# Optimization experiments

Measured on AMD Instinct MI355X. Metric: run time of the kernel, lower is better.

## Reference

```python
import jax, jax.numpy as jnp
import numpy as np


def setup_inputs() -> dict:
    key = jax.random.key(0)
    k1, k2, k3 = jax.random.split(key, 3)
    B, N, M, D = 4, 1024, 2048, 9
    outputs = jax.random.normal(k1, (B, N, D), dtype=jnp.float32)
    targets = jax.random.normal(k2, (B, M, D), dtype=jnp.float32)
    mask = jax.random.randint(k3, (B, M), 0, 2).astype(bool)
    return {"outputs": outputs, "targets": targets, "mask": mask, "k": 64, "max_pair": 1024}


def reference(outputs, targets, mask, k, max_pair):
    # outputs: (B, N, 9), targets: (B, M, 9), mask: (B, M) bool
    y_pred = outputs[:, :max_pair]
    B, N, D = y_pred.shape
    M = targets.shape[1]

    # Statistics over masked ground-truth rows (weighted, jit-friendly)
    w = mask.astype(y_pred.dtype)            # (B, M)
    S = w.sum()                               # number of valid rows
    mean = jnp.einsum('bm,bmd->d', w, targets) / S               # (9,)
    centered = (targets - mean) * w[..., None]                    # (B, M, 9)
    cov = jnp.einsum('bmd,bme->de', centered, centered) / (S - 1.0)
    cov_inv = jnp.linalg.pinv(cov)                                # (9, 9)

    def maha(x):
        # NOTE: original code subtracts the GT mean from the pairwise
        # differences before the quadratic form -- kept faithfully.
        xc = x - mean
        return jnp.einsum('...i,ij,...j->...', xc, cov_inv, xc)

    def topk_smallest_per_col(d, kk):
        # d: (R, N); torch.topk(dim=0, largest=False) -> smallest kk per column
        return -jax.lax.top_k(-d.T, kk)[0]    # (N, kk)

    # Intra loss: GT-vs-pred pairwise distances, masked rows only
    diff = targets[:, :, None, :] - y_pred[:, None, :, :]          # (B, M, N, 9)
    Dn = maha(diff)                                                 # (B, M, N)
    Dn = jnp.where(mask[:, :, None], Dn, jnp.inf).reshape(B * M, N)
    intra_loss = topk_smallest_per_col(Dn, k).mean()

    # Inter (regularization) loss: pred-vs-pred pairwise
    # y_reg1_expand[b,i,j] = y_pred[b,j]; y_reg2_expand[b,i,j] = y_pred[b,i]
    diff_r = y_pred[:, None, :, :] - y_pred[:, :, None, :]          # (B, N, N, 9)
    Dr = maha(diff_r).reshape(B * N, N)
    inter_loss = topk_smallest_per_col(Dr, k).mean()

    return intra_loss - 0.1 * inter_loss
```

## Files before the change

### kernel.cpp

```cpp
#include <hip/hip_runtime.h>
#include <math.h>

#define B_ 4
#define N_ 1024
#define M_ 2048
#define D_ 9
#define K_ 64
#define BM_ (B_*M_)
#define BN_ (B_*N_)
#define TPRE_STRIDE 12
#define PPRE_STRIDE 12
#define NPART 32
#define NSTAT 55
#define TSEL 512

#define WS_A 0
#define WS_MEAN 81
#define WS_TPRE 96
#define WS_PPRE (WS_TPRE + BM_*TPRE_STRIDE)
#define WS_CS_INTRA (WS_PPRE + BN_*PPRE_STRIDE)
#define WS_CS_INTER (WS_CS_INTRA + N_)
#define WS_PART (WS_CS_INTER + N_)
#define WS_CANDI (WS_PART + NPART*(NSTAT+1))
#define WS_CANDE (WS_CANDI + 1024*1024)

__device__ __forceinline__ unsigned f2key(float f) {
  unsigned b = __float_as_uint(f);
  return (b & 0x80000000u) ? ~b : (b | 0x80000000u);
}
__device__ __forceinline__ float key2f(unsigned k) {
  unsigned b = (k & 0x80000000u) ? (k ^ 0x80000000u) : ~k;
  return __uint_as_float(b);
}

__device__ int detect_mask_fmt(const void* mask, int* flags ) {
  int tid = threadIdx.x;
  if (tid < 2) flags[tid] = 0;
  __syncthreads();
  const unsigned char* mb = (const unsigned char*)mask;
  int la = 0, lb = 0;
  for (int i = tid; i < BM_; i += blockDim.x) {
    unsigned char c = mb[i];
    if (c) { if (i & 3) la = 1; else if ((i & 7) == 4) lb = 1; }
  }
  if (la) atomicOr(&flags[0], 1);
  if (lb) atomicOr(&flags[1], 1);
  __syncthreads();
  return flags[0] ? 0 : (flags[1] ? 1 : 2);
}
__device__ __forceinline__ int mask_at(const void* mask, int fmt, int t) {
  if (fmt == 0) return ((const unsigned char*)mask)[t] != 0;
  if (fmt == 1) return ((const int*)mask)[t] != 0;
  return ((const long long*)mask)[t] != 0LL;
}

__global__ __launch_bounds__(256) void stats_part_kernel(
    const float* __restrict__ targets, const void* __restrict__ mask,
    float* __restrict__ ws) {
  __shared__ int flags[2];
  __shared__ float wpart[4][NSTAT];
  int tid = threadIdx.x;
  int fmt = detect_mask_fmt(mask, flags);
  int t = blockIdx.x * 256 + tid;

  float v[NSTAT];
  float tv[D_];
  int m = mask_at(mask, fmt, t);
  const float* tp = targets + t * D_;
#pragma unroll
  for (int d = 0; d < D_; ++d) tv[d] = m ? tp[d] : 0.f;
  v[0] = m ? 1.f : 0.f;
#pragma unroll
  for (int d = 0; d < D_; ++d) v[1 + d] = tv[d];
  {
    int p = 10;
#pragma unroll
    for (int i = 0; i < D_; ++i)
#pragma unroll
      for (int j = i; j < D_; ++j, ++p) v[p] = tv[i] * tv[j];
  }
#pragma unroll
  for (int off = 32; off > 0; off >>= 1)
#pragma unroll
    for (int p = 0; p < NSTAT; ++p) v[p] += __shfl_down(v[p], off);
  int wave = tid >> 6, lane = tid & 63;
  if (lane == 0)
#pragma unroll
    for (int p = 0; p < NSTAT; ++p) wpart[wave][p] = v[p];
  __syncthreads();
  if (tid < NSTAT) {
    float s = wpart[0][tid] + wpart[1][tid] + wpart[2][tid] + wpart[3][tid];
    ws[WS_PART + blockIdx.x * (NSTAT + 1) + tid] = s;
  }
}

__global__ __launch_bounds__(64) void stats_fin_kernel(float* __restrict__ ws) {
  __shared__ float tot[NSTAT];
  __shared__ float Atmp[9][9];
  int lane = threadIdx.x;
  if (lane < NSTAT) {
    double s = 0.0;
    for (int b = 0; b < NPART; ++b)
      s += (double)ws[WS_PART + b * (NSTAT + 1) + lane];
    tot[lane] = (float)s;
  }
  __syncthreads();
  float S = tot[0];
  float col[9];
  int j = lane - 9;
  if (lane < 9) {
    float mj = tot[1 + lane] / S;
#pragma unroll
    for (int r = 0; r < 9; ++r) {
      float mr = tot[1 + r] / S;
      int i0 = r < lane ? r : lane;
      int j0 = r < lane ? lane : r;
      int p = i0 * 9 - (i0 * (i0 - 1)) / 2 + (j0 - i0);
      col[r] = (tot[10 + p] - S * mr * mj) / (S - 1.0f);
    }
  } else {
#pragma unroll
    for (int r = 0; r < 9; ++r) col[r] = (r == j) ? 1.f : 0.f;
  }
#pragma unroll
  for (int c = 0; c < 9; ++c) {
    float pv = __shfl(col[c], c);
    float inv = 1.f / pv;
    col[c] *= inv;
    float f[9];
#pragma unroll
    for (int r = 0; r < 9; ++r) f[r] = __shfl(col[r], c);
#pragma unroll
    for (int r = 0; r < 9; ++r)
      if (r != c) col[r] -= f[r] * col[c];
  }
  if (lane >= 9 && lane < 18) {
#pragma unroll
    for (int r = 0; r < 9; ++r) Atmp[r][j] = col[r];
  }
  __syncthreads();
  if (lane < 9) ws[WS_MEAN + lane] = tot[1 + lane] / S;
  for (int idx = lane; idx < 81; idx += 64) {
    int i0 = idx / 9, j0 = idx % 9;
    ws[WS_A + idx] = 0.5f * (Atmp[i0][j0] + Atmp[j0][i0]);
  }
}

__global__ __launch_bounds__(256) void pre_kernel(
    const float* __restrict__ outputs, const float* __restrict__ targets,
    const void* __restrict__ mask, float* __restrict__ ws) {
  __shared__ int flags[2];
  __shared__ float Ash[81];
  __shared__ float msh[D_];
  int tid = threadIdx.x;
  int fmt = detect_mask_fmt(mask, flags);
  if (tid < 81) Ash[tid] = ws[WS_A + tid];
  if (tid < D_) msh[tid] = ws[WS_MEAN + tid];
  __syncthreads();
  int idx = blockIdx.x * 256 + tid;
  if (idx < BM_) {
    const float* tp = targets + idx * D_;
    float u[D_];
#pragma unroll
    for (int d = 0; d < D_; ++d) u[d] = tp[d] - msh[d];
    float cu = 0.f; float au[D_];
#pragma unroll
    for (int i = 0; i < D_; ++i) {
      float s = 0.f;
#pragma unroll
      for (int j = 0; j < D_; ++j) s += Ash[i * D_ + j] * u[j];
      au[i] = s; cu += u[i] * s;
    }
    if (!mask_at(mask, fmt, idx)) cu = INFINITY;
    float* o = ws + WS_TPRE + idx * TPRE_STRIDE;
#pragma unroll
    for (int d = 0; d < D_; ++d) o[d] = au[d];
    o[9] = cu; o[10] = 0.f; o[11] = 0.f;
  } else if (idx < BM_ + BN_) {
    int r = idx - BM_;
    const float* yp = outputs + r * D_;
    float y[D_], q[D_], aq[D_];
#pragma unroll
    for (int d = 0; d < D_; ++d) { y[d] = yp[d]; q[d] = y[d] + msh[d]; }
    float cp = 0.f, cq = 0.f;
#pragma unroll
    for (int i = 0; i < D_; ++i) {
      float sy = 0.f, sq = 0.f;
#pragma unroll
      for (int j = 0; j < D_; ++j) {
        sy += Ash[i * D_ + j] * y[j];
        sq += Ash[i * D_ + j] * q[j];
      }
      cp += y[i] * sy;
      aq[i] = sq; cq += q[i] * sq;
    }
    float* o = ws + WS_PPRE + r * PPRE_STRIDE;
#pragma unroll
    for (int d = 0; d < D_; ++d) o[d] = aq[d];
    o[9] = cq; o[10] = cp; o[11] = 0.f;
  }
}

template <int PER>
__device__ __forceinline__ unsigned bisect64(const unsigned* key) {
  unsigned kmin = 0xFFFFFFFFu;
#pragma unroll
  for (int j = 0; j < PER; ++j) kmin = key[j] < kmin ? key[j] : kmin;
  unsigned gmin = kmin, mmax = kmin;
#pragma unroll
  for (int off = 32; off > 0; off >>= 1) {
    unsigned a = (unsigned)__shfl_xor((int)gmin, off);
    unsigned b = (unsigned)__shfl_xor((int)mmax, off);
    gmin = a < gmin ? a : gmin;
    mmax = b > mmax ? b : mmax;
  }
  unsigned lo = gmin, hi = mmax;
  while (lo < hi) {
    unsigned mid = lo + ((hi - lo) >> 1);
    int cnt = 0;
#pragma unroll
    for (int j = 0; j < PER; ++j) cnt += __popcll(__ballot(key[j] <= mid));
    if (cnt >= K_) hi = mid; else lo = mid + 1;
  }
  return lo;
}

template <int PER>
__device__ __forceinline__ void bisect64x2(const unsigned* k0,
                                           const unsigned* k1,
                                           unsigned& T0, unsigned& T1) {
  unsigned mn0 = 0xFFFFFFFFu, mn1 = 0xFFFFFFFFu;
#pragma unroll
  for (int j = 0; j < PER; ++j) {
    mn0 = k0[j] < mn0 ? k0[j] : mn0;
    mn1 = k1[j] < mn1 ? k1[j] : mn1;
  }
  unsigned g0 = mn0, x0 = mn0, g1 = mn1, x1 = mn1;
#pragma unroll
  for (int off = 32; off > 0; off >>= 1) {
    unsigned a0 = (unsigned)__shfl_xor((int)g0, off);
    unsigned b0 = (unsigned)__shfl_xor((int)x0, off);
    unsigned a1 = (unsigned)__shfl_xor((int)g1, off);
    unsigned b1 = (unsigned)__shfl_xor((int)x1, off);
    g0 = a0 < g0 ? a0 : g0;  x0 = b0 > x0 ? b0 : x0;
    g1 = a1 < g1 ? a1 : g1;  x1 = b1 > x1 ? b1 : x1;
  }
  unsigned lo0 = g0, hi0 = x0, lo1 = g1, hi1 = x1;
  while ((lo0 < hi0) || (lo1 < hi1)) {
    unsigned mid0 = lo0 + ((hi0 - lo0) >> 1);
    unsigned mid1 = lo1 + ((hi1 - lo1) >> 1);
    int c0 = 0, c1 = 0;
#pragma unroll
    for (int j = 0; j < PER; ++j) {
      c0 += __popcll(__ballot(k0[j] <= mid0));
      c1 += __popcll(__ballot(k1[j] <= mid1));
    }
    if (lo0 < hi0) { if (c0 >= K_) hi0 = mid0; else lo0 = mid0 + 1; }
    if (lo1 < hi1) { if (c1 >= K_) hi1 = mid1; else lo1 = mid1 + 1; }
  }
  T0 = lo0; T1 = lo1;
}

template <int PER>
__device__ __forceinline__ void compact64(const unsigned* key, unsigned T,
                                          float* candw, int lane) {
  unsigned long long lmask = (1ull << lane) - 1ull;
  int nlt = 0;
#pragma unroll
  for (int j = 0; j < PER; ++j) {
    bool p = key[j] < T;
    unsigned long long m = __ballot(p);
    if (p) candw[nlt + __popcll(m & lmask)] = key2f(key[j]);
    nlt += __popcll(m);
  }
  float tv = key2f(T);
  for (int i = nlt + lane; i < K_; i += 64) candw[i] = tv;
}

template <int NP>
__device__ __forceinline__ float final_sum(const float* __restrict__ cand,
                                           int lane) {
  float v[NP]; unsigned kk[NP];
#pragma unroll
  for (int j = 0; j < NP; ++j) {
    v[j] = cand[j * 64 + lane];
    kk[j] = f2key(v[j]);
  }
  unsigned T = bisect64<NP>(kk);
  float s = 0.f; int c = 0;
#pragma unroll
  for (int j = 0; j < NP; ++j)
    if (kk[j] < T) { s += v[j]; c++; }
#pragma unroll
  for (int off = 32; off > 0; off >>= 1) {
    s += __shfl_down(s, off);
    c += __shfl_down(c, off);
  }
  return s + (float)(K_ - c) * key2f(T);
}

__global__ __launch_bounds__(TSEL) void select_kernel(
    const float* __restrict__ outputs, const float* __restrict__ wsro,
    float* __restrict__ ws) {
  __shared__ float vsh[2][B_][D_];
  __shared__ float cvsh[2][B_];
  int tid = threadIdx.x, wave = tid >> 6, lane = tid & 63;
  int bid = blockIdx.x;
  int is_intra = bid < N_;
  int p = is_intra ? (bid >> 1) : (bid - N_);
  int h = is_intra ? (bid & 1) : 0;
  int c0 = 2 * p;
  if (tid < 2 * B_ * D_) {
    int c = tid / (B_ * D_), rem = tid % (B_ * D_), b = rem / D_, d = rem % D_;
    vsh[c][b][d] = outputs[(b * N_ + c0 + c) * D_ + d];
  }
  if (tid < 2 * B_) {
    int c = tid >> 2, b = tid & 3;
    cvsh[c][b] = wsro[WS_PPRE + (b * N_ + c0 + c) * PPRE_STRIDE + 10];
  }
  __syncthreads();
  constexpr int PER = 8;
  unsigned k0[PER], k1[PER];
  if (is_intra) {
    const float* pre = wsro + WS_TPRE;
    int rowbase = h * 4096;
#pragma unroll
    for (int bbb = 0; bbb < 2; ++bbb) {
      int b = 2 * h + bbb;
      float v0[D_], v1[D_];
#pragma unroll
      for (int d = 0; d < D_; ++d) { v0[d] = vsh[0][b][d]; v1[d] = vsh[1][b][d]; }
      float cv0 = cvsh[0][b], cv1 = cvsh[1][b];
#pragma unroll
      for (int jj = 0; jj < 4; ++jj) {
        int j = bbb * 4 + jj;
        const float* row = pre + (rowbase + tid + TSEL * j) * TPRE_STRIDE;
        float4 a0 = *(const float4*)row;
        float4 a1 = *(const float4*)(row + 4);
        float2 a2 = *(const float2*)(row + 8);
        float d0 = a0.x * v0[0] + a0.y * v0[1] + a0.z * v0[2] + a0.w * v0[3] +
                   a1.x * v0[4] + a1.y * v0[5] + a1.z * v0[6] + a1.w * v0[7] +
                   a2.x * v0[8];
        float d1 = a0.x * v1[0] + a0.y * v1[1] + a0.z * v1[2] + a0.w * v1[3] +
                   a1.x * v1[4] + a1.y * v1[5] + a1.z * v1[6] + a1.w * v1[7] +
                   a2.x * v1[8];
        k0[j] = f2key(a2.y + cv0 - 2.0f * d0);
        k1[j] = f2key(a2.y + cv1 - 2.0f * d1);
      }
      __builtin_amdgcn_sched_barrier(0);
    }
  } else {
    const float* pre = wsro + WS_PPRE;
#pragma unroll
    for (int bb = 0; bb < B_; ++bb) {
      float v0[D_], v1[D_];
#pragma unroll
      for (int d = 0; d < D_; ++d) { v0[d] = vsh[0][bb][d]; v1[d] = vsh[1][bb][d]; }
      float cv0 = cvsh[0][bb], cv1 = cvsh[1][bb];
#pragma unroll
      for (int jj = 0; jj < 2; ++jj) {
        int j = bb * 2 + jj;
        const float* row = pre + (tid + TSEL * j) * PPRE_STRIDE;
        float4 a0 = *(const float4*)row;
        float4 a1 = *(const float4*)(row + 4);
        float2 a2 = *(const float2*)(row + 8);
        float d0 = a0.x * v0[0] + a0.y * v0[1] + a0.z * v0[2] + a0.w * v0[3] +
                   a1.x * v0[4] + a1.y * v0[5] + a1.z * v0[6] + a1.w * v0[7] +
                   a2.x * v0[8];
        float d1 = a0.x * v1[0] + a0.y * v1[1] + a0.z * v1[2] + a0.w * v1[3] +
                   a1.x * v1[4] + a1.y * v1[5] + a1.z * v1[6] + a1.w * v1[7] +
                   a2.x * v1[8];
        k0[j] = f2key(a2.y + cv0 - 2.0f * d0);
        k1[j] = f2key(a2.y + cv1 - 2.0f * d1);
      }
      __builtin_amdgcn_sched_barrier(0);
    }
  }
  unsigned T0, T1;
  bisect64x2<PER>(k0, k1, T0, T1);
  if (is_intra) {
    float* base0 = ws + WS_CANDI + (c0) * 1024 + h * 512 + wave * 64;
    float* base1 = ws + WS_CANDI + (c0 + 1) * 1024 + h * 512 + wave * 64;
    compact64<PER>(k0, T0, base0, lane);
    compact64<PER>(k1, T1, base1, lane);
  } else {
    float* base0 = ws + WS_CANDE + (c0) * 512 + wave * 64;
    float* base1 = ws + WS_CANDE + (c0 + 1) * 512 + wave * 64;
    compact64<PER>(k0, T0, base0, lane);
    compact64<PER>(k1, T1, base1, lane);
  }
}

__global__ __launch_bounds__(512) void merge_kernel(
    const float* __restrict__ wsro, float* __restrict__ ws) {
  int gw = (blockIdx.x * 512 + threadIdx.x) >> 6;
  int lane = threadIdx.x & 63;
  if (gw < N_) {
    float s = final_sum<16>(wsro + WS_CANDI + gw * 1024, lane);
    if (lane == 0) ws[WS_CS_INTRA + gw] = s;
  } else {
    float s = final_sum<8>(wsro + WS_CANDE + (gw - N_) * 512, lane);
    if (lane == 0) ws[WS_CS_INTER + (gw - N_)] = s;
  }
}

__global__ __launch_bounds__(256) void reduce_kernel(
    const float* __restrict__ ws, float* __restrict__ out) {
  __shared__ double sbuf[256];
  __shared__ double tA;
  int tid = threadIdx.x;
  double sa = 0.0, sb = 0.0;
  for (int i = tid; i < N_; i += 256) {
    sa += (double)ws[WS_CS_INTRA + i];
    sb += (double)ws[WS_CS_INTER + i];
  }
  sbuf[tid] = sa;
  __syncthreads();
  for (int off = 128; off > 0; off >>= 1) {
    if (tid < off) sbuf[tid] += sbuf[tid + off];
    __syncthreads();
  }
  if (tid == 0) tA = sbuf[0];
  __syncthreads();
  sbuf[tid] = sb;
  __syncthreads();
  for (int off = 128; off > 0; off >>= 1) {
    if (tid < off) sbuf[tid] += sbuf[tid + off];
    __syncthreads();
  }
  if (tid == 0) {
    double denom = (double)N_ * (double)K_;
    out[0] = (float)(tA / denom - 0.1 * (sbuf[0] / denom));
  }
}

extern "C" void kernel_launch(void* const* d_in, const int* in_sizes, int n_in,
                              void* d_out, int out_size, void* d_ws,
                              size_t ws_size, hipStream_t stream) {
  const float* outputs = (const float*)d_in[0];
  const float* targets = (const float*)d_in[1];
  const void* mask = d_in[2];
  float* ws = (float*)d_ws;

  hipLaunchKernelGGL(stats_part_kernel, dim3(NPART), dim3(256), 0, stream,
                     targets, mask, ws);
  hipLaunchKernelGGL(stats_fin_kernel, dim3(1), dim3(64), 0, stream, ws);
  hipLaunchKernelGGL(pre_kernel, dim3((BM_ + BN_ + 255) / 256), dim3(256), 0,
                     stream, outputs, targets, mask, ws);
  hipLaunchKernelGGL(select_kernel, dim3(N_ + N_ / 2), dim3(TSEL), 0, stream,
                     outputs, ws, ws);
  hipLaunchKernelGGL(merge_kernel, dim3(2 * N_ / 8), dim3(512), 0, stream,
                     ws, ws);
  hipLaunchKernelGGL(reduce_kernel, dim3(1), dim3(256), 0, stream, ws,
                     (float*)d_out);
}
```

Before: 75.84 us.

## Fuse covariance inverse into pre kernel and use early-exit bisection budget

Removes the single-block stats_fin launch by having every pre_kernel block redundantly compute the covariance inverse and mean from the partial sums. The per-wave threshold bisection now stops once at most 128 candidates lie at or below the threshold, instead of bisecting exactly to the 64th value. This cuts bisection iterations in the select kernel at the cost of writing twice as many candidates and doubling the work in the merge kernel. Redundant per-block inversion adds some latency to every pre block.

```diff
diff --git a/kernel.cpp b/kernel.cpp
--- a/kernel.cpp
+++ b/kernel.cpp
@@ -13,6 +13,7 @@
 #define NPART 32
 #define NSTAT 55
 #define TSEL 512
+#define BUD 128
 
 #define WS_A 0
 #define WS_MEAN 81
@@ -22,7 +23,7 @@
 #define WS_CS_INTER (WS_CS_INTRA + N_)
 #define WS_PART (WS_CS_INTER + N_)
 #define WS_CANDI (WS_PART + NPART*(NSTAT+1))
-#define WS_CANDE (WS_CANDI + 1024*1024)
+#define WS_CANDE (WS_CANDI + 1024*2048)
 
 __device__ __forceinline__ unsigned f2key(float f) {
   unsigned b = __float_as_uint(f);
@@ -94,69 +95,67 @@
   }
 }
 
-__global__ __launch_bounds__(64) void stats_fin_kernel(float* __restrict__ ws) {
-  __shared__ float tot[NSTAT];
-  __shared__ float Atmp[9][9];
-  int lane = threadIdx.x;
-  if (lane < NSTAT) {
-    double s = 0.0;
-    for (int b = 0; b < NPART; ++b)
-      s += (double)ws[WS_PART + b * (NSTAT + 1) + lane];
-    tot[lane] = (float)s;
-  }
-  __syncthreads();
-  float S = tot[0];
-  float col[9];
-  int j = lane - 9;
-  if (lane < 9) {
-    float mj = tot[1 + lane] / S;
-#pragma unroll
-    for (int r = 0; r < 9; ++r) {
-      float mr = tot[1 + r] / S;
-      int i0 = r < lane ? r : lane;
-      int j0 = r < lane ? lane : r;
-      int p = i0 * 9 - (i0 * (i0 - 1)) / 2 + (j0 - i0);
-      col[r] = (tot[10 + p] - S * mr * mj) / (S - 1.0f);
-    }
-  } else {
-#pragma unroll
-    for (int r = 0; r < 9; ++r) col[r] = (r == j) ? 1.f : 0.f;
-  }
-#pragma unroll
-  for (int c = 0; c < 9; ++c) {
-    float pv = __shfl(col[c], c);
-    float inv = 1.f / pv;
-    col[c] *= inv;
-    float f[9];
-#pragma unroll
-    for (int r = 0; r < 9; ++r) f[r] = __shfl(col[r], c);
-#pragma unroll
-    for (int r = 0; r < 9; ++r)
-      if (r != c) col[r] -= f[r] * col[c];
-  }
-  if (lane >= 9 && lane < 18) {
-#pragma unroll
-    for (int r = 0; r < 9; ++r) Atmp[r][j] = col[r];
-  }
-  __syncthreads();
-  if (lane < 9) ws[WS_MEAN + lane] = tot[1 + lane] / S;
-  for (int idx = lane; idx < 81; idx += 64) {
-    int i0 = idx / 9, j0 = idx % 9;
-    ws[WS_A + idx] = 0.5f * (Atmp[i0][j0] + Atmp[j0][i0]);
-  }
-}
-
 __global__ __launch_bounds__(256) void pre_kernel(
     const float* __restrict__ outputs, const float* __restrict__ targets,
     const void* __restrict__ mask, float* __restrict__ ws) {
   __shared__ int flags[2];
+  __shared__ float tot[NSTAT];
+  __shared__ float Atmp[9][9];
   __shared__ float Ash[81];
   __shared__ float msh[D_];
   int tid = threadIdx.x;
   int fmt = detect_mask_fmt(mask, flags);
-  if (tid < 81) Ash[tid] = ws[WS_A + tid];
-  if (tid < D_) msh[tid] = ws[WS_MEAN + tid];
-  __syncthreads();
+  if (tid < NSTAT) {
+    double s = 0.0;
+    for (int b = 0; b < NPART; ++b)
+      s += (double)ws[WS_PART + b * (NSTAT + 1) + tid];
+    tot[tid] = (float)s;
+  }
+  __syncthreads();
+  if (tid < 64) {
+    int lane = tid;
+    float S = tot[0];
+    float col[9];
+    int j = lane - 9;
+    if (lane < 9) {
+      float mj = tot[1 + lane] / S;
+#pragma unroll
+      for (int r = 0; r < 9; ++r) {
+        float mr = tot[1 + r] / S;
+        int i0 = r < lane ? r : lane;
+        int j0 = r < lane ? lane : r;
+        int p = i0 * 9 - (i0 * (i0 - 1)) / 2 + (j0 - i0);
+        col[r] = (tot[10 + p] - S * mr * mj) / (S - 1.0f);
+      }
+    } else {
+#pragma unroll
+      for (int r = 0; r < 9; ++r) col[r] = (r == j) ? 1.f : 0.f;
+    }
+#pragma unroll
+    for (int c = 0; c < 9; ++c) {
+      float pv = __shfl(col[c], c);
+      float inv = 1.f / pv;
+      col[c] *= inv;
+      float f[9];
+#pragma unroll
+      for (int r = 0; r < 9; ++r) f[r] = __shfl(col[r], c);
+#pragma unroll
+      for (int r = 0; r < 9; ++r)
+        if (r != c) col[r] -= f[r] * col[c];
+    }
+    if (lane >= 9 && lane < 18) {
+#pragma unroll
+      for (int r = 0; r < 9; ++r) Atmp[r][j] = col[r];
+    }
+  }
+  __syncthreads();
+  if (tid < 9) msh[tid] = tot[1 + tid] / tot[0];
+  for (int idx = tid; idx < 81; idx += 256) {
+    int i0 = idx / 9, j0 = idx % 9;
+    Ash[idx] = 0.5f * (Atmp[i0][j0] + Atmp[j0][i0]);
+  }
+  __syncthreads();
+
   int idx = blockIdx.x * 256 + tid;
   if (idx < BM_) {
     const float* tp = targets + idx * D_;
@@ -226,9 +225,10 @@
 }
 
 template <int PER>
-__device__ __forceinline__ void bisect64x2(const unsigned* k0,
-                                           const unsigned* k1,
-                                           unsigned& T0, unsigned& T1) {
+__device__ __forceinline__ void sel_thresh2(const unsigned* k0,
+                                            const unsigned* k1,
+                                            unsigned& T0o, unsigned& T1o,
+                                            int& st0, int& st1) {
   unsigned mn0 = 0xFFFFFFFFu, mn1 = 0xFFFFFFFFu;
 #pragma unroll
   for (int j = 0; j < PER; ++j) {
@@ -246,51 +246,57 @@
     g1 = a1 < g1 ? a1 : g1;  x1 = b1 > x1 ? b1 : x1;
   }
   unsigned lo0 = g0, hi0 = x0, lo1 = g1, hi1 = x1;
-  while ((lo0 < hi0) || (lo1 < hi1)) {
+  int c0 = 0, c1 = 0;
+#pragma unroll
+  for (int j = 0; j < PER; ++j) {
+    c0 += __popcll(__ballot(k0[j] <= hi0));
+    c1 += __popcll(__ballot(k1[j] <= hi1));
+  }
+  while (((lo0 < hi0) && (c0 > BUD)) || ((lo1 < hi1) && (c1 > BUD))) {
+    int a0 = (lo0 < hi0) && (c0 > BUD);
+    int a1 = (lo1 < hi1) && (c1 > BUD);
     unsigned mid0 = lo0 + ((hi0 - lo0) >> 1);
     unsigned mid1 = lo1 + ((hi1 - lo1) >> 1);
-    int c0 = 0, c1 = 0;
+    int n0 = 0, n1 = 0;
 #pragma unroll
     for (int j = 0; j < PER; ++j) {
-      c0 += __popcll(__ballot(k0[j] <= mid0));
-      c1 += __popcll(__ballot(k1[j] <= mid1));
-    }
-    if (lo0 < hi0) { if (c0 >= K_) hi0 = mid0; else lo0 = mid0 + 1; }
-    if (lo1 < hi1) { if (c1 >= K_) hi1 = mid1; else lo1 = mid1 + 1; }
-  }
-  T0 = lo0; T1 = lo1;
+      n0 += __popcll(__ballot(k0[j] <= mid0));
+      n1 += __popcll(__ballot(k1[j] <= mid1));
+    }
+    if (a0) { if (n0 >= K_) { hi0 = mid0; c0 = n0; } else lo0 = mid0 + 1; }
+    if (a1) { if (n1 >= K_) { hi1 = mid1; c1 = n1; } else lo1 = mid1 + 1; }
+  }
+  T0o = hi0; st0 = (c0 > BUD);
+  T1o = hi1; st1 = (c1 > BUD);
 }
 
 template <int PER>
-__device__ __forceinline__ void compact64(const unsigned* key, unsigned T,
-                                          float* candw, int lane) {
+__device__ __forceinline__ void compactB(const unsigned* key, unsigned T,
+                                         int strict, float* candw, int lane) {
   unsigned long long lmask = (1ull << lane) - 1ull;
-  int nlt = 0;
+  int n = 0;
 #pragma unroll
   for (int j = 0; j < PER; ++j) {
-    bool p = key[j] < T;
+    bool p = strict ? (key[j] < T) : (key[j] <= T);
     unsigned long long m = __ballot(p);
-    if (p) candw[nlt + __popcll(m & lmask)] = key2f(key[j]);
-    nlt += __popcll(m);
+    if (p) candw[n + __popcll(m & lmask)] = key2f(key[j]);
+    n += __popcll(m);
   }
   float tv = key2f(T);
-  for (int i = nlt + lane; i < K_; i += 64) candw[i] = tv;
+  for (int i = n + lane; i < BUD; i += 64) candw[i] = tv;
 }
 
 template <int NP>
 __device__ __forceinline__ float final_sum(const float* __restrict__ cand,
                                            int lane) {
-  float v[NP]; unsigned kk[NP];
-#pragma unroll
-  for (int j = 0; j < NP; ++j) {
-    v[j] = cand[j * 64 + lane];
-    kk[j] = f2key(v[j]);
-  }
+  unsigned kk[NP];
+#pragma unroll
+  for (int j = 0; j < NP; ++j) kk[j] = f2key(cand[j * 64 + lane]);
   unsigned T = bisect64<NP>(kk);
   float s = 0.f; int c = 0;
 #pragma unroll
   for (int j = 0; j < NP; ++j)
-    if (kk[j] < T) { s += v[j]; c++; }
+    if (kk[j] < T) { s += key2f(kk[j]); c++; }
 #pragma unroll
   for (int off = 32; off > 0; off >>= 1) {
     s += __shfl_down(s, off);
@@ -376,18 +382,18 @@
       __builtin_amdgcn_sched_barrier(0);
     }
   }
-  unsigned T0, T1;
-  bisect64x2<PER>(k0, k1, T0, T1);
+  unsigned T0, T1; int st0, st1;
+  sel_thresh2<PER>(k0, k1, T0, T1, st0, st1);
   if (is_intra) {
-    float* base0 = ws + WS_CANDI + (c0) * 1024 + h * 512 + wave * 64;
-    float* base1 = ws + WS_CANDI + (c0 + 1) * 1024 + h * 512 + wave * 64;
-    compact64<PER>(k0, T0, base0, lane);
-    compact64<PER>(k1, T1, base1, lane);
+    compactB<PER>(k0, T0, st0,
+                  ws + WS_CANDI + (c0) * 2048 + h * 1024 + wave * BUD, lane);
+    compactB<PER>(k1, T1, st1,
+                  ws + WS_CANDI + (c0 + 1) * 2048 + h * 1024 + wave * BUD, lane);
   } else {
-    float* base0 = ws + WS_CANDE + (c0) * 512 + wave * 64;
-    float* base1 = ws + WS_CANDE + (c0 + 1) * 512 + wave * 64;
-    compact64<PER>(k0, T0, base0, lane);
-    compact64<PER>(k1, T1, base1, lane);
+    compactB<PER>(k0, T0, st0,
+                  ws + WS_CANDE + (c0) * 1024 + wave * BUD, lane);
+    compactB<PER>(k1, T1, st1,
+                  ws + WS_CANDE + (c0 + 1) * 1024 + wave * BUD, lane);
   }
 }
 
@@ -396,10 +402,10 @@
   int gw = (blockIdx.x * 512 + threadIdx.x) >> 6;
   int lane = threadIdx.x & 63;
   if (gw < N_) {
-    float s = final_sum<16>(wsro + WS_CANDI + gw * 1024, lane);
+    float s = final_sum<32>(wsro + WS_CANDI + gw * 2048, lane);
     if (lane == 0) ws[WS_CS_INTRA + gw] = s;
   } else {
-    float s = final_sum<8>(wsro + WS_CANDE + (gw - N_) * 512, lane);
+    float s = final_sum<16>(wsro + WS_CANDE + (gw - N_) * 1024, lane);
     if (lane == 0) ws[WS_CS_INTER + (gw - N_)] = s;
   }
 }
@@ -444,7 +450,6 @@
 
   hipLaunchKernelGGL(stats_part_kernel, dim3(NPART), dim3(256), 0, stream,
                      targets, mask, ws);
-  hipLaunchKernelGGL(stats_fin_kernel, dim3(1), dim3(64), 0, stream, ws);
   hipLaunchKernelGGL(pre_kernel, dim3((BM_ + BN_ + 255) / 256), dim3(256), 0,
                      stream, outputs, targets, mask, ws);
   hipLaunchKernelGGL(select_kernel, dim3(N_ + N_ / 2), dim3(TSEL), 0, stream,
```

Measured after the change: 70.79 us. -6.7%, faster.
